# Performance work log

Measured on AMD Instinct MI355X. Metric: run time of the kernel, lower is better.

Reference implementation:

```python
import jax, jax.numpy as jnp
import numpy as np

EPS = 1e-7  # tf.keras.backend.epsilon()
ROUTINGS = 3


def squash(s):
    # s: [B, J, D]
    n2 = jnp.sum(s * s, axis=-1, keepdims=True) + EPS
    return (n2 / (1.0 + n2)) * s / jnp.sqrt(n2)


def setup_inputs() -> dict:
    key = jax.random.key(0)
    k1, k2 = jax.random.split(key)
    B, I, P = 64, 2048, 16   # batch, input_num_capsules, input_dim_capsules
    J, D = 32, 16            # num_capsules, dim_capsules (must equal P per source matmul)
    inputs = jax.random.normal(k1, (B, I, P), dtype=jnp.float32)
    W = jax.random.normal(k2, (I, J, P, D), dtype=jnp.float32) * 0.05  # glorot-ish scale
    return {"inputs": inputs, "W": W}


def reference(inputs, W):
    # tf.matmul(W_tiled, inputs_tiled): u_hat[b,i,j,d] = sum_p W[i,j,d,p] * inputs[b,i,p]
    u_hat = jnp.einsum('bip,ijdp->bijd', inputs, W)  # [B, I, J, D]
    B, I, J, _ = u_hat.shape
    b = jnp.zeros((B, I, J), dtype=u_hat.dtype)
    v = None
    for r in range(ROUTINGS):
        c = jax.nn.softmax(b, axis=2)                  # [B, I, J]
        s = jnp.einsum('bij,bijd->bjd', c, u_hat)      # [B, J, D]
        v = squash(s)
        if r < ROUTINGS - 1:
            b = b + jnp.einsum('bijd,bjd->bij', u_hat, v)
    return v
```

## Files before the change

### kernel.cpp

```cpp
#include <hip/hip_runtime.h>
#include <hip/hip_bf16.h>
#include <stdint.h>


namespace {
constexpr int B_ = 64;
constexpr int I_ = 2048;
constexpr int P_ = 16;
constexpr int J_ = 32;
constexpr int D_ = 16;
constexpr int CI_ = 128;
constexpr int NBLK_ = I_ / CI_;
constexpr int ROWS_ = J_ * D_;

using half8 = __attribute__((ext_vector_type(8))) _Float16;
using h2    = __attribute__((ext_vector_type(2))) _Float16;
using f32x4 = __attribute__((ext_vector_type(4))) float;

__device__ __forceinline__ uint32_t pkh2(float a, float b) {
  union { h2 h; uint32_t u; } z;
  z.h[0] = (_Float16)a; z.h[1] = (_Float16)b;
  return z.u;
}
__device__ __forceinline__ h2 as_h2(uint32_t u) {
  union { uint32_t uu; h2 h; } z; z.uu = u; return z.h;
}
__device__ __forceinline__ float dot2acc(h2 a, h2 b, float c) {
#if __has_builtin(__builtin_amdgcn_fdot2)
  return __builtin_amdgcn_fdot2(a, b, c, false);
#else
  return fmaf((float)a[0], (float)b[0], fmaf((float)a[1], (float)b[1], c));
#endif
}

__global__ __launch_bounds__(256) void k_uhat(const float* __restrict__ x,
                                              const float* __restrict__ W,
                                              uint16_t* __restrict__ uhat) {
  const int i = blockIdx.x;
  const int t = threadIdx.x;
  const int w = t >> 6;
  const int l = t & 63;
  const int g = l >> 4;
  const int r16 = l & 15;

  half8 bfr[4];
#pragma unroll
  for (int bm = 0; bm < 4; ++bm) {
    half8 f;
#pragma unroll
    for (int e = 0; e < 8; ++e) f[e] = (_Float16)0.f;
    if (g < 2) {
      const float* bp = x + (size_t)(16 * bm + r16) * (I_ * P_) + (size_t)i * P_ + 8 * g;
      const float4 u0 = *reinterpret_cast<const float4*>(bp);
      const float4 u1 = *reinterpret_cast<const float4*>(bp + 4);
      f[0] = (_Float16)u0.x; f[1] = (_Float16)u0.y; f[2] = (_Float16)u0.z; f[3] = (_Float16)u0.w;
      f[4] = (_Float16)u1.x; f[5] = (_Float16)u1.y; f[6] = (_Float16)u1.z; f[7] = (_Float16)u1.w;
    }
    bfr[bm] = f;
  }

  const float* Wi = W + (size_t)i * (ROWS_ * P_);
  uint16_t* out_i = uhat + (size_t)i * (B_ * ROWS_);

#pragma unroll
  for (int nn = 0; nn < 8; ++nn) {
    const int n = 8 * w + nn;
    half8 af;
#pragma unroll
    for (int e = 0; e < 8; ++e) af[e] = (_Float16)0.f;
    if (g < 2) {
      const float* ap = Wi + (size_t)(16 * n + r16) * P_ + 8 * g;
      const float4 u0 = *reinterpret_cast<const float4*>(ap);
      const float4 u1 = *reinterpret_cast<const float4*>(ap + 4);
      af[0] = (_Float16)u0.x; af[1] = (_Float16)u0.y; af[2] = (_Float16)u0.z; af[3] = (_Float16)u0.w;
      af[4] = (_Float16)u1.x; af[5] = (_Float16)u1.y; af[6] = (_Float16)u1.z; af[7] = (_Float16)u1.w;
    }

#pragma unroll
    for (int bm = 0; bm < 4; ++bm) {
      f32x4 acc;
      acc[0] = 0.f; acc[1] = 0.f; acc[2] = 0.f; acc[3] = 0.f;
      acc = __builtin_amdgcn_mfma_f32_16x16x32_f16(af, bfr[bm], acc, 0, 0, 0);
      const int b = 16 * bm + r16;
      const int ro = 16 * n + 4 * g;
      uint2 st;
      st.x = pkh2(acc[0], acc[1]);
      st.y = pkh2(acc[2], acc[3]);
      *reinterpret_cast<uint2*>(out_i + (size_t)b * ROWS_ + ro) = st;
    }
  }
}

template <bool UNIFORM>
__global__ __launch_bounds__(256) void k_route(const uint4* __restrict__ uhat,
                                               const float* __restrict__ vsum,
                                               float* __restrict__ part) {
  const int b = blockIdx.y;
  const int i0 = blockIdx.x * CI_;
  const int t = threadIdx.x;
  const int lane = t & 63;
  const int wave = t >> 6;
  const int sub = lane >> 5;
  const int j = lane & 31;

  h2 vh[8];
  if constexpr (!UNIFORM) {
    const float4* vp = reinterpret_cast<const float4*>(vsum + ((size_t)b * J_ + j) * D_);
#pragma unroll
    for (int q = 0; q < 4; ++q) {
      const float4 v = vp[q];
      h2 a, bb;
      a[0] = (_Float16)v.x; a[1] = (_Float16)v.y;
      bb[0] = (_Float16)v.z; bb[1] = (_Float16)v.w;
      vh[2 * q] = a; vh[2 * q + 1] = bb;
    }
  }

  float acc[D_];
#pragma unroll
  for (int d = 0; d < D_; ++d) acc[d] = 0.f;

  const uint4* up = uhat + ((size_t)(i0 + wave * 2 + sub) * B_ + b) * (ROWS_ / 8) + j * 2;
  const size_t step = (size_t)8 * B_ * (ROWS_ / 8);

#pragma unroll 2
  for (int it = 0; it < CI_ / 8; ++it, up += step) {
    const uint4 q0 = up[0], q1 = up[1];
    const h2 u0 = as_h2(q0.x), u1 = as_h2(q0.y), u2 = as_h2(q0.z), u3 = as_h2(q0.w);
    const h2 u4 = as_h2(q1.x), u5 = as_h2(q1.y), u6 = as_h2(q1.z), u7 = as_h2(q1.w);
    float c;
    if constexpr (UNIFORM) {
      c = 1.0f;
    } else {
      float lg = 0.f;
      lg = dot2acc(u0, vh[0], lg); lg = dot2acc(u1, vh[1], lg);
      lg = dot2acc(u2, vh[2], lg); lg = dot2acc(u3, vh[3], lg);
      lg = dot2acc(u4, vh[4], lg); lg = dot2acc(u5, vh[5], lg);
      lg = dot2acc(u6, vh[6], lg); lg = dot2acc(u7, vh[7], lg);
      const float e = __expf(lg);
      float sm = e;
#pragma unroll
      for (int off = 16; off > 0; off >>= 1) sm += __shfl_xor(sm, off, 32);
      c = e * __builtin_amdgcn_rcpf(sm);
    }
    acc[0]  = fmaf((float)u0[0], c, acc[0]);  acc[1]  = fmaf((float)u0[1], c, acc[1]);
    acc[2]  = fmaf((float)u1[0], c, acc[2]);  acc[3]  = fmaf((float)u1[1], c, acc[3]);
    acc[4]  = fmaf((float)u2[0], c, acc[4]);  acc[5]  = fmaf((float)u2[1], c, acc[5]);
    acc[6]  = fmaf((float)u3[0], c, acc[6]);  acc[7]  = fmaf((float)u3[1], c, acc[7]);
    acc[8]  = fmaf((float)u4[0], c, acc[8]);  acc[9]  = fmaf((float)u4[1], c, acc[9]);
    acc[10] = fmaf((float)u5[0], c, acc[10]); acc[11] = fmaf((float)u5[1], c, acc[11]);
    acc[12] = fmaf((float)u6[0], c, acc[12]); acc[13] = fmaf((float)u6[1], c, acc[13]);
    acc[14] = fmaf((float)u7[0], c, acc[14]); acc[15] = fmaf((float)u7[1], c, acc[15]);
  }
  if constexpr (UNIFORM) {
#pragma unroll
    for (int d = 0; d < D_; ++d) acc[d] *= (1.0f / J_);
  }
#pragma unroll
  for (int d = 0; d < D_; ++d) acc[d] += __shfl_xor(acc[d], 32, 64);

  __shared__ float sp[4][J_][D_ + 1];
  if (sub == 0) {
#pragma unroll
    for (int d = 0; d < D_; ++d) sp[wave][j][d] = acc[d];
  }
  __syncthreads();
  float* dst = part + ((size_t)b * NBLK_ + blockIdx.x) * (J_ * D_);
  for (int k = t; k < J_ * D_; k += 256) {
    const int jj = k >> 4, dd = k & 15;
    dst[k] = sp[0][jj][dd] + sp[1][jj][dd] + sp[2][jj][dd] + sp[3][jj][dd];
  }
}

template <bool ADD_PREV, bool TO_OUT>
__global__ __launch_bounds__(256) void k_finish(const float* __restrict__ part,
                                                float* __restrict__ vsum,
                                                float* __restrict__ out) {
  const int b = blockIdx.x;
  const int t = threadIdx.x;
  const float* pb = part + (size_t)b * NBLK_ * (J_ * D_);
  float slo = 0.f, shi = 0.f;
#pragma unroll
  for (int blk = 0; blk < NBLK_; ++blk) {
    slo += pb[blk * (J_ * D_) + t];
    shi += pb[blk * (J_ * D_) + t + 256];
  }
  float nlo = slo * slo, nhi = shi * shi;
#pragma unroll
  for (int off = 8; off > 0; off >>= 1) {
    nlo += __shfl_xor(nlo, off, 16);
    nhi += __shfl_xor(nhi, off, 16);
  }
  nlo += 1e-7f; nhi += 1e-7f;
  const float sclo = nlo / ((1.f + nlo) * sqrtf(nlo));
  const float schi = nhi / ((1.f + nhi) * sqrtf(nhi));
  const float vlo = sclo * slo, vhi = schi * shi;
  if constexpr (TO_OUT) {
    out[(size_t)b * (J_ * D_) + t] = vlo;
    out[(size_t)b * (J_ * D_) + t + 256] = vhi;
  } else {
    float plo = 0.f, phi = 0.f;
    if constexpr (ADD_PREV) {
      plo = vsum[(size_t)b * (J_ * D_) + t];
      phi = vsum[(size_t)b * (J_ * D_) + t + 256];
    }
    vsum[(size_t)b * (J_ * D_) + t] = plo + vlo;
    vsum[(size_t)b * (J_ * D_) + t + 256] = phi + vhi;
  }
}

}

extern "C" void kernel_launch(void* const* d_in, const int* in_sizes, int n_in,
                              void* d_out, int out_size, void* d_ws, size_t ws_size,
                              hipStream_t stream) {
  const float* x = (const float*)d_in[0];
  const float* W = (const float*)d_in[1];
  float* out = (float*)d_out;

  char* ws = (char*)d_ws;
  uint16_t* uhat = (uint16_t*)ws;
  const size_t UHAT_BYTES = (size_t)I_ * B_ * ROWS_ * 2;
  float* part = (float*)(ws + UHAT_BYTES);
  float* vsum = part + (size_t)B_ * NBLK_ * (J_ * D_);

  k_uhat<<<I_, 256, 0, stream>>>(x, W, uhat);

  const dim3 rg(NBLK_, B_);
  k_route<true><<<rg, 256, 0, stream>>>((const uint4*)uhat, nullptr, part);
  k_finish<false, false><<<B_, 256, 0, stream>>>(part, vsum, nullptr);
  k_route<false><<<rg, 256, 0, stream>>>((const uint4*)uhat, vsum, part);
  k_finish<true, false><<<B_, 256, 0, stream>>>(part, vsum, nullptr);
  k_route<false><<<rg, 256, 0, stream>>>((const uint4*)uhat, vsum, part);
  k_finish<false, true><<<B_, 256, 0, stream>>>(part, nullptr, out);
}
```

Baseline: 263.1 us.

## Stage uhat stores through LDS and fold squash reduction into routing kernels

The uhat kernel now writes MFMA results into a swizzled shared-memory tile and then emits fully coalesced 16-byte global stores, replacing scattered 8-byte stores. The separate finish kernels are removed: each routing pass recomputes the partial-sum reduction and squash for its batch row at block start, keeping separate partial buffers per pass. This cuts four launches and the vsum round trip, but every route block redundantly re-reduces the partials. The routing loop unroll is also raised from 2 to 4.

```diff
diff --git a/kernel.cpp b/kernel.cpp
--- a/kernel.cpp
+++ b/kernel.cpp
@@ -43,6 +43,8 @@
   const int g = l >> 4;
   const int r16 = l & 15;
 
+  __shared__ uint16_t sbuf[B_ * ROWS_];
+
   half8 bfr[4];
 #pragma unroll
   for (int bm = 0; bm < 4; ++bm) {
@@ -60,7 +62,6 @@
   }
 
   const float* Wi = W + (size_t)i * (ROWS_ * P_);
-  uint16_t* out_i = uhat + (size_t)i * (B_ * ROWS_);
 
 #pragma unroll
   for (int nn = 0; nn < 8; ++nn) {
@@ -83,18 +84,51 @@
       acc = __builtin_amdgcn_mfma_f32_16x16x32_f16(af, bfr[bm], acc, 0, 0, 0);
       const int b = 16 * bm + r16;
       const int ro = 16 * n + 4 * g;
+      const int idx = b * ROWS_ + (ro ^ ((b & 14) << 2));
       uint2 st;
       st.x = pkh2(acc[0], acc[1]);
       st.y = pkh2(acc[2], acc[3]);
-      *reinterpret_cast<uint2*>(out_i + (size_t)b * ROWS_ + ro) = st;
-    }
-  }
-}
-
-template <bool UNIFORM>
+      *reinterpret_cast<uint2*>(&sbuf[idx]) = st;
+    }
+  }
+
+  __syncthreads();
+
+  uint16_t* out_i = uhat + (size_t)i * (B_ * ROWS_);
+#pragma unroll
+  for (int k = 0; k < 16; ++k) {
+    const int b = 4 * k + w;
+    const int ro = l * 8;
+    const int c = (b & 14) << 2;
+    const uint4 v = *reinterpret_cast<const uint4*>(&sbuf[b * ROWS_ + (ro ^ c)]);
+    *reinterpret_cast<uint4*>(&out_i[b * ROWS_ + ro]) = v;
+  }
+}
+
+__device__ __forceinline__ void accum_squash(const float* __restrict__ pb, int tk,
+                                             float& vlo, float& vhi) {
+  float slo = 0.f, shi = 0.f;
+#pragma unroll
+  for (int blk = 0; blk < NBLK_; ++blk) {
+    slo += pb[blk * (J_ * D_) + tk];
+    shi += pb[blk * (J_ * D_) + tk + 256];
+  }
+  float nlo = slo * slo, nhi = shi * shi;
+#pragma unroll
+  for (int off = 8; off > 0; off >>= 1) {
+    nlo += __shfl_xor(nlo, off, 16);
+    nhi += __shfl_xor(nhi, off, 16);
+  }
+  nlo += 1e-7f; nhi += 1e-7f;
+  vlo += slo * (nlo / ((1.f + nlo) * sqrtf(nlo)));
+  vhi += shi * (nhi / ((1.f + nhi) * sqrtf(nhi)));
+}
+
+template <int PASS>
 __global__ __launch_bounds__(256) void k_route(const uint4* __restrict__ uhat,
-                                               const float* __restrict__ vsum,
-                                               float* __restrict__ part) {
+                                               const float* __restrict__ part0,
+                                               const float* __restrict__ part1,
+                                               float* __restrict__ part_out) {
   const int b = blockIdx.y;
   const int i0 = blockIdx.x * CI_;
   const int t = threadIdx.x;
@@ -103,16 +137,22 @@
   const int sub = lane >> 5;
   const int j = lane & 31;
 
+  __shared__ float vlds[J_][D_ + 1];
   h2 vh[8];
-  if constexpr (!UNIFORM) {
-    const float4* vp = reinterpret_cast<const float4*>(vsum + ((size_t)b * J_ + j) * D_);
-#pragma unroll
-    for (int q = 0; q < 4; ++q) {
-      const float4 v = vp[q];
-      h2 a, bb;
-      a[0] = (_Float16)v.x; a[1] = (_Float16)v.y;
-      bb[0] = (_Float16)v.z; bb[1] = (_Float16)v.w;
-      vh[2 * q] = a; vh[2 * q + 1] = bb;
+  if constexpr (PASS > 0) {
+    float vlo = 0.f, vhi = 0.f;
+    accum_squash(part0 + (size_t)b * NBLK_ * (J_ * D_), t, vlo, vhi);
+    if constexpr (PASS == 2)
+      accum_squash(part1 + (size_t)b * NBLK_ * (J_ * D_), t, vlo, vhi);
+    vlds[t >> 4][t & 15] = vlo;
+    vlds[16 + (t >> 4)][t & 15] = vhi;
+    __syncthreads();
+#pragma unroll
+    for (int q = 0; q < 8; ++q) {
+      h2 hv;
+      hv[0] = (_Float16)vlds[j][2 * q];
+      hv[1] = (_Float16)vlds[j][2 * q + 1];
+      vh[q] = hv;
     }
   }
 
@@ -123,13 +163,13 @@
   const uint4* up = uhat + ((size_t)(i0 + wave * 2 + sub) * B_ + b) * (ROWS_ / 8) + j * 2;
   const size_t step = (size_t)8 * B_ * (ROWS_ / 8);
 
-#pragma unroll 2
+#pragma unroll 4
   for (int it = 0; it < CI_ / 8; ++it, up += step) {
     const uint4 q0 = up[0], q1 = up[1];
     const h2 u0 = as_h2(q0.x), u1 = as_h2(q0.y), u2 = as_h2(q0.z), u3 = as_h2(q0.w);
     const h2 u4 = as_h2(q1.x), u5 = as_h2(q1.y), u6 = as_h2(q1.z), u7 = as_h2(q1.w);
     float c;
-    if constexpr (UNIFORM) {
+    if constexpr (PASS == 0) {
       c = 1.0f;
     } else {
       float lg = 0.f;
@@ -152,7 +192,7 @@
     acc[12] = fmaf((float)u6[0], c, acc[12]); acc[13] = fmaf((float)u6[1], c, acc[13]);
     acc[14] = fmaf((float)u7[0], c, acc[14]); acc[15] = fmaf((float)u7[1], c, acc[15]);
   }
-  if constexpr (UNIFORM) {
+  if constexpr (PASS == 0) {
 #pragma unroll
     for (int d = 0; d < D_; ++d) acc[d] *= (1.0f / J_);
   }
@@ -165,48 +205,21 @@
     for (int d = 0; d < D_; ++d) sp[wave][j][d] = acc[d];
   }
   __syncthreads();
-  float* dst = part + ((size_t)b * NBLK_ + blockIdx.x) * (J_ * D_);
+  float* dst = part_out + ((size_t)b * NBLK_ + blockIdx.x) * (J_ * D_);
   for (int k = t; k < J_ * D_; k += 256) {
     const int jj = k >> 4, dd = k & 15;
     dst[k] = sp[0][jj][dd] + sp[1][jj][dd] + sp[2][jj][dd] + sp[3][jj][dd];
   }
 }
 
-template <bool ADD_PREV, bool TO_OUT>
-__global__ __launch_bounds__(256) void k_finish(const float* __restrict__ part,
-                                                float* __restrict__ vsum,
-                                                float* __restrict__ out) {
+__global__ __launch_bounds__(256) void k_out(const float* __restrict__ part2,
+                                             float* __restrict__ out) {
   const int b = blockIdx.x;
   const int t = threadIdx.x;
-  const float* pb = part + (size_t)b * NBLK_ * (J_ * D_);
-  float slo = 0.f, shi = 0.f;
-#pragma unroll
-  for (int blk = 0; blk < NBLK_; ++blk) {
-    slo += pb[blk * (J_ * D_) + t];
-    shi += pb[blk * (J_ * D_) + t + 256];
-  }
-  float nlo = slo * slo, nhi = shi * shi;
-#pragma unroll
-  for (int off = 8; off > 0; off >>= 1) {
-    nlo += __shfl_xor(nlo, off, 16);
-    nhi += __shfl_xor(nhi, off, 16);
-  }
-  nlo += 1e-7f; nhi += 1e-7f;
-  const float sclo = nlo / ((1.f + nlo) * sqrtf(nlo));
-  const float schi = nhi / ((1.f + nhi) * sqrtf(nhi));
-  const float vlo = sclo * slo, vhi = schi * shi;
-  if constexpr (TO_OUT) {
-    out[(size_t)b * (J_ * D_) + t] = vlo;
-    out[(size_t)b * (J_ * D_) + t + 256] = vhi;
-  } else {
-    float plo = 0.f, phi = 0.f;
-    if constexpr (ADD_PREV) {
-      plo = vsum[(size_t)b * (J_ * D_) + t];
-      phi = vsum[(size_t)b * (J_ * D_) + t + 256];
-    }
-    vsum[(size_t)b * (J_ * D_) + t] = plo + vlo;
-    vsum[(size_t)b * (J_ * D_) + t + 256] = phi + vhi;
-  }
+  float vlo = 0.f, vhi = 0.f;
+  accum_squash(part2 + (size_t)b * NBLK_ * (J_ * D_), t, vlo, vhi);
+  out[(size_t)b * (J_ * D_) + t] = vlo;
+  out[(size_t)b * (J_ * D_) + t + 256] = vhi;
 }
 
 }
@@ -221,16 +234,15 @@
   char* ws = (char*)d_ws;
   uint16_t* uhat = (uint16_t*)ws;
   const size_t UHAT_BYTES = (size_t)I_ * B_ * ROWS_ * 2;
-  float* part = (float*)(ws + UHAT_BYTES);
-  float* vsum = part + (size_t)B_ * NBLK_ * (J_ * D_);
+  float* part0 = (float*)(ws + UHAT_BYTES);
+  float* part1 = part0 + (size_t)B_ * NBLK_ * (J_ * D_);
+  float* part2 = part1 + (size_t)B_ * NBLK_ * (J_ * D_);
 
   k_uhat<<<I_, 256, 0, stream>>>(x, W, uhat);
 
   const dim3 rg(NBLK_, B_);
-  k_route<true><<<rg, 256, 0, stream>>>((const uint4*)uhat, nullptr, part);
-  k_finish<false, false><<<B_, 256, 0, stream>>>(part, vsum, nullptr);
-  k_route<false><<<rg, 256, 0, stream>>>((const uint4*)uhat, vsum, part);
-  k_finish<true, false><<<B_, 256, 0, stream>>>(part, vsum, nullptr);
-  k_route<false><<<rg, 256, 0, stream>>>((const uint4*)uhat, vsum, part);
-  k_finish<false, true><<<B_, 256, 0, stream>>>(part, nullptr, out);
-}
+  k_route<0><<<rg, 256, 0, stream>>>((const uint4*)uhat, nullptr, nullptr, part0);
+  k_route<1><<<rg, 256, 0, stream>>>((const uint4*)uhat, part0, nullptr, part1);
+  k_route<2><<<rg, 256, 0, stream>>>((const uint4*)uhat, part0, part1, part2);
+  k_out<<<B_, 256, 0, stream>>>(part2, out);
+}
```

Result: faster. 214.8 us (-18.4%).
